# Optimization experiments

Hardware: AMD Instinct MI355X
Metric: run time of the kernel (lower is better)

The kernel has to match this reference:

```python
import jax, jax.numpy as jnp
import numpy as np

EPS = 1e-7
K = 15      # kernel_size
CIN = 128
F = 256


def setup_inputs() -> dict:
    key = jax.random.key(0)
    k1, k2 = jax.random.split(key)
    x = jax.random.normal(k1, (32, 4096, CIN), dtype=jnp.float32)
    # glorot-uniform init then UnitNorm over axes (0,1) per filter, matching the constraint
    limit = np.sqrt(6.0 / (K * CIN + F))
    kernel = jax.random.uniform(k2, (K, CIN, F), dtype=jnp.float32, minval=-limit, maxval=limit)
    kernel = kernel / jnp.sqrt(jnp.sum(kernel * kernel, axis=(0, 1), keepdims=True) + 1e-12)
    scale = jnp.full((1, 1, 1), 10.0, dtype=jnp.float32)
    bias = jnp.zeros((F,), dtype=jnp.float32)
    return {"inputs": x, "kernel": kernel, "scale": scale, "bias": bias}


def reference(inputs, kernel, scale, bias):
    # dot-product conv: (B, L-K+1, F), VALID padding, stride 1
    dot = jax.lax.conv_general_dilated(
        inputs, kernel, window_strides=(1,), padding="VALID",
        dimension_numbers=("NWC", "WIO", "NWC"))
    # sliding sum-of-squares over window*channels. In the original this is a
    # conv1d with an all-ones (K,CIN,F) kernel, i.e. every filter sees the same
    # scalar sum -> compute it once via a cumsum box filter and broadcast.
    k = kernel.shape[0]
    sq = jnp.sum(inputs * inputs, axis=-1)                       # (B, L)
    cs = jnp.cumsum(jnp.pad(sq, ((0, 0), (1, 0))), axis=1)       # (B, L+1)
    win = cs[:, k:] - cs[:, :-k]                                 # (B, L-K+1)
    norm_x = jnp.sqrt(win + EPS)[..., None]                      # (B, L-K+1, 1)
    return scale * (dot / norm_x) + bias
```

## Files before the change

### kernel.cpp

```cpp
#include <hip/hip_runtime.h>
#include <hip/hip_bf16.h>
#include <stdint.h>

#define K_TAPS 15
#define CIN    128
#define F_OUT  256
#define LSEQ   4096
#define LOUT   (LSEQ - K_TAPS + 1)
#define BATCH  32

typedef __attribute__((ext_vector_type(8))) short bf16x8;
typedef __attribute__((ext_vector_type(4))) float f32x4;

typedef __attribute__((address_space(1))) const unsigned int gu32_t;
typedef __attribute__((address_space(3))) unsigned int su32_t;

__global__ void prep_w_kernel(const float* __restrict__ W,
                              unsigned short* __restrict__ Wp) {
  int idx = blockIdx.x * 256 + threadIdx.x;
  int f  = idx & 255;
  int kc = idx >> 8;
  int c  = kc & 127;
  int k  = kc >> 7;
  float w = W[idx];
  __hip_bfloat16 hb = __float2bfloat16(w);
  int chalf = c >> 6;
  int c6    = c & 63;
  int slot  = ((c6 >> 3) ^ f) & 7;
  int cp    = slot * 8 + (c & 7);
  Wp[((size_t)(k * 2 + chalf) * 256 + f) * 64 + cp] =
      *reinterpret_cast<unsigned short*>(&hb);
}

__global__ void sq_kernel(const float* __restrict__ x, float* __restrict__ sq) {
  int wid  = threadIdx.x >> 6;
  int lane = threadIdx.x & 63;
  int half = lane >> 5;
  int lq   = lane & 31;
  long pos = (long)blockIdx.x * 8 + wid * 2 + half;
  const float4* xp = (const float4*)(x + pos * CIN) + lq;
  float4 v = *xp;
  float s = v.x * v.x + v.y * v.y + v.z * v.z + v.w * v.w;
  #pragma unroll
  for (int m = 1; m <= 16; m <<= 1) s += __shfl_xor(s, m, 64);
  if (lq == 0) sq[pos] = s;
}

__global__ void rn_kernel(const float* __restrict__ sq,
                          const float* __restrict__ scale,
                          float* __restrict__ rn) {
  int t = blockIdx.x * 256 + threadIdx.x;
  int b = blockIdx.y;
  if (t >= LOUT) return;
  const float* s = sq + b * LSEQ + t;
  float w = 0.f;
  #pragma unroll
  for (int k = 0; k < K_TAPS; ++k) w += s[k];
  rn[b * LSEQ + t] = scale[0] / sqrtf(w + 1e-7f);
}

#define BM 128
#define BN 128
#define XROWS 144
#define XBYTES (XROWS * 256)
#define BBYTES 16384
#define NPHASE (K_TAPS * 2)

__global__ __launch_bounds__(256, 2) void conv_gemm_kernel(
    const float* __restrict__ x, const unsigned short* __restrict__ Wp,
    const float* __restrict__ rn, const float* __restrict__ bias,
    float* __restrict__ out)
{
  __shared__ __align__(16) char lds[XBYTES + 2 * BBYTES];
  char* Xs = lds;
  char* Bs = lds + XBYTES;

  const int b     = blockIdx.y;
  const int mtile = blockIdx.x >> 1;
  const int ntile = blockIdx.x & 1;
  const int t0    = mtile * BM;
  const int n0    = ntile * BN;

  const int tx   = threadIdx.x;
  const int wid  = tx >> 6;
  const int lane = tx & 63;
  const int wm   = wid >> 1;
  const int wn   = wid & 1;

  {
    const int rloc = tx >> 4;
    const int g    = tx & 15;
    const float* xb = x + (long)b * LSEQ * CIN;
    #pragma unroll
    for (int it = 0; it < 9; ++it) {
      int row  = it * 16 + rloc;
      int grow = t0 + row;
      float v[8];
      if (grow < LSEQ) {
        const float4* p = (const float4*)(xb + (long)grow * CIN + g * 8);
        float4 a0 = p[0], a1 = p[1];
        v[0]=a0.x; v[1]=a0.y; v[2]=a0.z; v[3]=a0.w;
        v[4]=a1.x; v[5]=a1.y; v[6]=a1.z; v[7]=a1.w;
      } else {
        #pragma unroll
        for (int j = 0; j < 8; ++j) v[j] = 0.f;
      }
      union { unsigned short us[8]; int4 q; } pk;
      #pragma unroll
      for (int j = 0; j < 8; ++j) {
        __hip_bfloat16 hb = __float2bfloat16(v[j]);
        pk.us[j] = *reinterpret_cast<unsigned short*>(&hb);
      }
      int slot = (g & 8) | ((g ^ row) & 7);
      *(int4*)(Xs + row * 256 + slot * 16) = pk.q;
    }
  }

  auto stageB = [&](int buf, int phase) {
    const char* src = (const char*)Wp + (size_t)phase * 32768
                      + (size_t)n0 * 128;
    char* dst = Bs + buf * BBYTES;
    int base = wid * 4096;
    #pragma unroll
    for (int i = 0; i < 4; ++i) {
      int off = base + i * 1024;
      __builtin_amdgcn_global_load_lds(
          (gu32_t*)(src + off + lane * 16),
          (su32_t*)(dst + off), 16, 0, 0);
    }
  };

  stageB(0, 0);
  __syncthreads();

  f32x4 acc[4][4] = {};

  const int klane = lane >> 4;
  const int rl    = lane & 15;
  const int arow0 = wm * 64;
  const int bcol0 = wn * 64;

  for (int ph = 0; ph < NPHASE; ++ph) {
    int buf = ph & 1;
    if (ph + 1 < NPHASE) stageB(buf ^ 1, ph + 1);
    const char* Bsc = Bs + buf * BBYTES;
    const int tap = ph >> 1;
    const int kk0 = (ph & 1) * 2;
    #pragma unroll
    for (int j = 0; j < 2; ++j) {
      const int kk = kk0 + j;
      bf16x8 af[4], bfr[4];
      const int ga = kk * 4 + klane;
      const int gb = (kk & 1) * 4 + klane;
      #pragma unroll
      for (int mf = 0; mf < 4; ++mf) {
        int row  = arow0 + mf * 16 + rl + tap;
        int slot = (ga & 8) | ((ga ^ row) & 7);
        af[mf] = *(const bf16x8*)(Xs + row * 256 + slot * 16);
      }
      #pragma unroll
      for (int nf = 0; nf < 4; ++nf) {
        int fc   = bcol0 + nf * 16 + rl;
        int slot = (gb ^ fc) & 7;
        bfr[nf] = *(const bf16x8*)(Bsc + fc * 128 + slot * 16);
      }
      #pragma unroll
      for (int mf = 0; mf < 4; ++mf)
        #pragma unroll
        for (int nf = 0; nf < 4; ++nf)
          acc[mf][nf] = __builtin_amdgcn_mfma_f32_16x16x32_bf16(
              af[mf], bfr[nf], acc[mf][nf], 0, 0, 0);
    }
    __syncthreads();
  }

  const int rgrp = lane >> 4;
  float biasv[4];
  #pragma unroll
  for (int nf = 0; nf < 4; ++nf) biasv[nf] = bias[n0 + bcol0 + nf * 16 + rl];
  float* ob = out + (long)b * LOUT * F_OUT;
  const float* rnb = rn + b * LSEQ + t0;
  #pragma unroll
  for (int mf = 0; mf < 4; ++mf) {
    #pragma unroll
    for (int r = 0; r < 4; ++r) {
      int row = arow0 + mf * 16 + rgrp * 4 + r;
      int gt  = t0 + row;
      if (gt < LOUT) {
        float rv = rnb[row];
        #pragma unroll
        for (int nf = 0; nf < 4; ++nf) {
          ob[(long)gt * F_OUT + n0 + bcol0 + nf * 16 + rl] =
              acc[mf][nf][r] * rv + biasv[nf];
        }
      }
    }
  }
}

extern "C" void kernel_launch(void* const* d_in, const int* in_sizes, int n_in,
                              void* d_out, int out_size, void* d_ws, size_t ws_size,
                              hipStream_t stream) {
  const float* x     = (const float*)d_in[0];
  const float* W     = (const float*)d_in[1];
  const float* scale = (const float*)d_in[2];
  const float* bias  = (const float*)d_in[3];
  float* out = (float*)d_out;

  char* ws = (char*)d_ws;
  unsigned short* Wp = (unsigned short*)ws;
  float* sq = (float*)(ws + 1048576);
  float* rn = (float*)(ws + 1048576 + 524288);

  prep_w_kernel<<<1920, 256, 0, stream>>>(W, Wp);
  sq_kernel<<<BATCH * LSEQ / 8, 256, 0, stream>>>(x, sq);
  rn_kernel<<<dim3((LOUT + 255) / 256, BATCH), 256, 0, stream>>>(sq, scale, rn);
  conv_gemm_kernel<<<dim3(64, BATCH), 256, 0, stream>>>(x, Wp, rn, bias, out);
}
```

Baseline: 148.9 us.

## Load weight fragments directly from global into registers, drop LDS staging

Changes the packed-weight layout so each lane's MFMA B fragment is a contiguous 16-byte global load. Weights now go straight into registers with a two-phase register double buffer, instead of being staged through double-buffered LDS with per-phase barriers. This removes the per-phase __syncthreads and the B LDS traffic, and shrinks LDS so occupancy can rise to 3 blocks per SM. The cost is more register pressure and exposed global or L2 latency on the weight loads, which every wave now issues redundantly.

```diff
diff --git a/kernel.cpp b/kernel.cpp
--- a/kernel.cpp
+++ b/kernel.cpp
@@ -11,9 +11,6 @@
 
 typedef __attribute__((ext_vector_type(8))) short bf16x8;
 typedef __attribute__((ext_vector_type(4))) float f32x4;
-
-typedef __attribute__((address_space(1))) const unsigned int gu32_t;
-typedef __attribute__((address_space(3))) unsigned int su32_t;
 
 __global__ void prep_w_kernel(const float* __restrict__ W,
                               unsigned short* __restrict__ Wp) {
@@ -24,12 +21,11 @@
   int k  = kc >> 7;
   float w = W[idx];
   __hip_bfloat16 hb = __float2bfloat16(w);
-  int chalf = c >> 6;
-  int c6    = c & 63;
-  int slot  = ((c6 >> 3) ^ f) & 7;
-  int cp    = slot * 8 + (c & 7);
-  Wp[((size_t)(k * 2 + chalf) * 256 + f) * 64 + cp] =
-      *reinterpret_cast<unsigned short*>(&hb);
+  int kk = c >> 5;
+  int kl = (c >> 3) & 3;
+  int c7 = c & 7;
+  size_t o = ((((size_t)(k * 4 + kk) * 256 + f) * 4 + kl) * 8) + c7;
+  Wp[o] = *reinterpret_cast<unsigned short*>(&hb);
 }
 
 __global__ void sq_kernel(const float* __restrict__ x, float* __restrict__ sq) {
@@ -60,32 +56,33 @@
 }
 
 #define BM 128
-#define BN 128
 #define XROWS 144
 #define XBYTES (XROWS * 256)
-#define BBYTES 16384
 #define NPHASE (K_TAPS * 2)
 
-__global__ __launch_bounds__(256, 2) void conv_gemm_kernel(
+__global__ __launch_bounds__(256, 3) void conv_gemm_kernel(
     const float* __restrict__ x, const unsigned short* __restrict__ Wp,
     const float* __restrict__ rn, const float* __restrict__ bias,
     float* __restrict__ out)
 {
-  __shared__ __align__(16) char lds[XBYTES + 2 * BBYTES];
-  char* Xs = lds;
-  char* Bs = lds + XBYTES;
+  __shared__ __align__(16) char Xs[XBYTES];
 
   const int b     = blockIdx.y;
   const int mtile = blockIdx.x >> 1;
   const int ntile = blockIdx.x & 1;
   const int t0    = mtile * BM;
-  const int n0    = ntile * BN;
+  const int n0    = ntile * 128;
 
   const int tx   = threadIdx.x;
   const int wid  = tx >> 6;
   const int lane = tx & 63;
   const int wm   = wid >> 1;
   const int wn   = wid & 1;
+
+  const int klane = lane >> 4;
+  const int rl    = lane & 15;
+  const int arow0 = wm * 64;
+  const int bcol0 = wn * 64;
 
   {
     const int rloc = tx >> 4;
@@ -115,43 +112,33 @@
       *(int4*)(Xs + row * 256 + slot * 16) = pk.q;
     }
   }
-
-  auto stageB = [&](int buf, int phase) {
-    const char* src = (const char*)Wp + (size_t)phase * 32768
-                      + (size_t)n0 * 128;
-    char* dst = Bs + buf * BBYTES;
-    int base = wid * 4096;
-    #pragma unroll
-    for (int i = 0; i < 4; ++i) {
-      int off = base + i * 1024;
-      __builtin_amdgcn_global_load_lds(
-          (gu32_t*)(src + off + lane * 16),
-          (su32_t*)(dst + off), 16, 0, 0);
-    }
-  };
-
-  stageB(0, 0);
   __syncthreads();
 
-  f32x4 acc[4][4] = {};
-
-  const int klane = lane >> 4;
-  const int rl    = lane & 15;
-  const int arow0 = wm * 64;
-  const int bcol0 = wn * 64;
-
-  for (int ph = 0; ph < NPHASE; ++ph) {
-    int buf = ph & 1;
-    if (ph + 1 < NPHASE) stageB(buf ^ 1, ph + 1);
-    const char* Bsc = Bs + buf * BBYTES;
+  const char* wbase = (const char*)Wp
+      + (size_t)(n0 + bcol0 + rl) * 64 + (size_t)klane * 16;
+  auto loadB = [&](int ph, bf16x8* br) {
     const int tap = ph >> 1;
     const int kk0 = (ph & 1) * 2;
     #pragma unroll
     for (int j = 0; j < 2; ++j) {
+      const char* base = wbase + (size_t)((tap * 4 + kk0 + j) * 256) * 64;
+      #pragma unroll
+      for (int nf = 0; nf < 4; ++nf) {
+        br[j * 4 + nf] = *(const bf16x8*)(base + (size_t)nf * 16 * 64);
+      }
+    }
+  };
+
+  f32x4 acc[4][4] = {};
+
+  auto compute = [&](int ph, const bf16x8* br) {
+    const int tap = ph >> 1;
+    const int kk0 = (ph & 1) * 2;
+    #pragma unroll
+    for (int j = 0; j < 2; ++j) {
       const int kk = kk0 + j;
-      bf16x8 af[4], bfr[4];
       const int ga = kk * 4 + klane;
-      const int gb = (kk & 1) * 4 + klane;
+      bf16x8 af[4];
       #pragma unroll
       for (int mf = 0; mf < 4; ++mf) {
         int row  = arow0 + mf * 16 + rl + tap;
@@ -159,19 +146,22 @@
         af[mf] = *(const bf16x8*)(Xs + row * 256 + slot * 16);
       }
       #pragma unroll
-      for (int nf = 0; nf < 4; ++nf) {
-        int fc   = bcol0 + nf * 16 + rl;
-        int slot = (gb ^ fc) & 7;
-        bfr[nf] = *(const bf16x8*)(Bsc + fc * 128 + slot * 16);
-      }
-      #pragma unroll
       for (int mf = 0; mf < 4; ++mf)
         #pragma unroll
         for (int nf = 0; nf < 4; ++nf)
           acc[mf][nf] = __builtin_amdgcn_mfma_f32_16x16x32_bf16(
-              af[mf], bfr[nf], acc[mf][nf], 0, 0, 0);
-    }
-    __syncthreads();
+              af[mf], br[j * 4 + nf], acc[mf][nf], 0, 0, 0);
+    }
+  };
+
+  bf16x8 bA[8], bB[8];
+  loadB(0, bA);
+  #pragma unroll 3
+  for (int ph = 0; ph < NPHASE; ph += 2) {
+    loadB(ph + 1, bB);
+    compute(ph, bA);
+    if (ph + 2 < NPHASE) loadB(ph + 2, bA);
+    compute(ph + 1, bB);
   }
 
   const int rgrp = lane >> 4;
```

Result: slower. 169.2 us (+13.6%).

## Overlap weight prefetch with MFMA using manual vmcnt waits and split barriers

Applied to the files above, without the earlier changes.

Replaces the per-phase __syncthreads with explicit s_waitcnt vmcnt(4) and s_barrier, so the next phase's weight tile prefetch into LDS can stay in flight while the current phase's MFMAs run. The first weight-tile load is now issued before the input tile is converted to bf16 and staged, hiding its latency. A-fragment reads are hoisted ahead of the barrier, MFMAs are wrapped in s_setprio, and the phase loop is unrolled by 2. This relies on correct manual waitcnt accounting for the async LDS loads, which makes it fragile if the number of loads per stage changes.

```diff
diff --git a/kernel.cpp b/kernel.cpp
--- a/kernel.cpp
+++ b/kernel.cpp
@@ -87,6 +87,22 @@
   const int wm   = wid >> 1;
   const int wn   = wid & 1;
 
+  auto stageB = [&](int buf, int phase) {
+    const char* src = (const char*)Wp + (size_t)phase * 32768
+                      + (size_t)n0 * 128;
+    char* dst = Bs + buf * BBYTES;
+    int base = wid * 4096;
+    #pragma unroll
+    for (int i = 0; i < 4; ++i) {
+      int off = base + i * 1024;
+      __builtin_amdgcn_global_load_lds(
+          (gu32_t*)(src + off + lane * 16),
+          (su32_t*)(dst + off), 16, 0, 0);
+    }
+  };
+
+  stageB(0, 0);
+
   {
     const int rloc = tx >> 4;
     const int g    = tx & 15;
@@ -115,22 +131,6 @@
       *(int4*)(Xs + row * 256 + slot * 16) = pk.q;
     }
   }
-
-  auto stageB = [&](int buf, int phase) {
-    const char* src = (const char*)Wp + (size_t)phase * 32768
-                      + (size_t)n0 * 128;
-    char* dst = Bs + buf * BBYTES;
-    int base = wid * 4096;
-    #pragma unroll
-    for (int i = 0; i < 4; ++i) {
-      int off = base + i * 1024;
-      __builtin_amdgcn_global_load_lds(
-          (gu32_t*)(src + off + lane * 16),
-          (su32_t*)(dst + off), 16, 0, 0);
-    }
-  };
-
-  stageB(0, 0);
   __syncthreads();
 
   f32x4 acc[4][4] = {};
@@ -140,38 +140,59 @@
   const int arow0 = wm * 64;
   const int bcol0 = wn * 64;
 
+  #pragma unroll 2
   for (int ph = 0; ph < NPHASE; ++ph) {
-    int buf = ph & 1;
-    if (ph + 1 < NPHASE) stageB(buf ^ 1, ph + 1);
-    const char* Bsc = Bs + buf * BBYTES;
+    const int buf = ph & 1;
     const int tap = ph >> 1;
     const int kk0 = (ph & 1) * 2;
+
+    if (ph + 1 < NPHASE) stageB(buf ^ 1, ph + 1);
+
+    bf16x8 af[2][4];
     #pragma unroll
     for (int j = 0; j < 2; ++j) {
-      const int kk = kk0 + j;
-      bf16x8 af[4], bfr[4];
-      const int ga = kk * 4 + klane;
-      const int gb = (kk & 1) * 4 + klane;
+      const int ga = (kk0 + j) * 4 + klane;
       #pragma unroll
       for (int mf = 0; mf < 4; ++mf) {
         int row  = arow0 + mf * 16 + rl + tap;
         int slot = (ga & 8) | ((ga ^ row) & 7);
-        af[mf] = *(const bf16x8*)(Xs + row * 256 + slot * 16);
-      }
+        af[j][mf] = *(const bf16x8*)(Xs + row * 256 + slot * 16);
+      }
+    }
+
+    if (ph + 1 < NPHASE) {
+      asm volatile("s_waitcnt vmcnt(4)" ::: "memory");
+    } else {
+      asm volatile("s_waitcnt vmcnt(0)" ::: "memory");
+    }
+    __builtin_amdgcn_s_barrier();
+
+    const char* Bsc = Bs + buf * BBYTES;
+    bf16x8 bfr[2][4];
+    #pragma unroll
+    for (int j = 0; j < 2; ++j) {
+      const int gb = ((kk0 + j) & 1) * 4 + klane;
       #pragma unroll
       for (int nf = 0; nf < 4; ++nf) {
         int fc   = bcol0 + nf * 16 + rl;
         int slot = (gb ^ fc) & 7;
-        bfr[nf] = *(const bf16x8*)(Bsc + fc * 128 + slot * 16);
-      }
+        bfr[j][nf] = *(const bf16x8*)(Bsc + fc * 128 + slot * 16);
+      }
+    }
+
+    __builtin_amdgcn_s_setprio(1);
+    #pragma unroll
+    for (int j = 0; j < 2; ++j)
       #pragma unroll
       for (int mf = 0; mf < 4; ++mf)
         #pragma unroll
         for (int nf = 0; nf < 4; ++nf)
           acc[mf][nf] = __builtin_amdgcn_mfma_f32_16x16x32_bf16(
-              af[mf], bfr[nf], acc[mf][nf], 0, 0, 0);
-    }
-    __syncthreads();
+              af[j][mf], bfr[j][nf], acc[mf][nf], 0, 0, 0);
+    __builtin_amdgcn_s_setprio(0);
+
+    asm volatile("s_waitcnt lgkmcnt(0)" ::: "memory");
+    __builtin_amdgcn_s_barrier();
   }
 
   const int rgrp = lane >> 4;
```

New measurement: 147.5 us, median of 2. No clear change (-0.9%).

## Halve weight stage size, add manual waitcnt barriers and raise occupancy

Applied to the files above, without the earlier changes.

Repacks the bf16 weights into 32-channel quarter-phases with a new 4-slot XOR swizzle, halving each LDS B buffer and doubling the phase count. The main loop now issues the next weight prefetch, loads A fragments before waiting, and uses explicit vmcnt/lgkmcnt waits plus raw s_barrier instead of __syncthreads. It also raises MFMA priority with s_setprio and asks for 3 blocks per CU, and the first weight prefetch is issued before the x tile is converted so the two overlap. The aim is to hide global-to-LDS latency and improve occupancy. The cost is twice as many barriers per tap and a hand-tuned wait count that must match the number of outstanding loads.

```diff
diff --git a/kernel.cpp b/kernel.cpp
--- a/kernel.cpp
+++ b/kernel.cpp
@@ -24,11 +24,11 @@
   int k  = kc >> 7;
   float w = W[idx];
   __hip_bfloat16 hb = __float2bfloat16(w);
-  int chalf = c >> 6;
-  int c6    = c & 63;
-  int slot  = ((c6 >> 3) ^ f) & 7;
-  int cp    = slot * 8 + (c & 7);
-  Wp[((size_t)(k * 2 + chalf) * 256 + f) * 64 + cp] =
+  int q    = c >> 5;
+  int g    = (c >> 3) & 3;
+  int slot = (g ^ f ^ (f >> 2)) & 3;
+  int cp   = slot * 8 + (c & 7);
+  Wp[((size_t)(k * 4 + q) * 256 + f) * 32 + cp] =
       *reinterpret_cast<unsigned short*>(&hb);
 }
 
@@ -63,10 +63,10 @@
 #define BN 128
 #define XROWS 144
 #define XBYTES (XROWS * 256)
-#define BBYTES 16384
-#define NPHASE (K_TAPS * 2)
-
-__global__ __launch_bounds__(256, 2) void conv_gemm_kernel(
+#define BBYTES 8192
+#define NPHASE (K_TAPS * 4)
+
+__global__ __launch_bounds__(256, 3) void conv_gemm_kernel(
     const float* __restrict__ x, const unsigned short* __restrict__ Wp,
     const float* __restrict__ rn, const float* __restrict__ bias,
     float* __restrict__ out)
@@ -86,6 +86,22 @@
   const int lane = tx & 63;
   const int wm   = wid >> 1;
   const int wn   = wid & 1;
+
+  auto stageB = [&](int buf, int phase) {
+    const char* src = (const char*)Wp + (size_t)phase * 16384
+                      + (size_t)n0 * 64;
+    char* dst = Bs + buf * BBYTES;
+    int base = wid * 2048;
+    #pragma unroll
+    for (int i = 0; i < 2; ++i) {
+      int off = base + i * 1024;
+      __builtin_amdgcn_global_load_lds(
+          (gu32_t*)(src + off + lane * 16),
+          (su32_t*)(dst + off), 16, 0, 0);
+    }
+  };
+
+  stageB(0, 0);
 
   {
     const int rloc = tx >> 4;
@@ -115,22 +131,6 @@
       *(int4*)(Xs + row * 256 + slot * 16) = pk.q;
     }
   }
-
-  auto stageB = [&](int buf, int phase) {
-    const char* src = (const char*)Wp + (size_t)phase * 32768
-                      + (size_t)n0 * 128;
-    char* dst = Bs + buf * BBYTES;
-    int base = wid * 4096;
-    #pragma unroll
-    for (int i = 0; i < 4; ++i) {
-      int off = base + i * 1024;
-      __builtin_amdgcn_global_load_lds(
-          (gu32_t*)(src + off + lane * 16),
-          (su32_t*)(dst + off), 16, 0, 0);
-    }
-  };
-
-  stageB(0, 0);
   __syncthreads();
 
   f32x4 acc[4][4] = {};
@@ -140,38 +140,50 @@
   const int arow0 = wm * 64;
   const int bcol0 = wn * 64;
 
+  #pragma unroll 4
   for (int ph = 0; ph < NPHASE; ++ph) {
-    int buf = ph & 1;
+    const int buf = ph & 1;
+    const int tap = ph >> 2;
+    const int qtr = ph & 3;
+
     if (ph + 1 < NPHASE) stageB(buf ^ 1, ph + 1);
+
+    const int ga = qtr * 4 + klane;
+    bf16x8 af[4];
+    #pragma unroll
+    for (int mf = 0; mf < 4; ++mf) {
+      int row  = arow0 + mf * 16 + rl + tap;
+      int slot = (ga & 8) | ((ga ^ row) & 7);
+      af[mf] = *(const bf16x8*)(Xs + row * 256 + slot * 16);
+    }
+
+    if (ph + 1 < NPHASE) {
+      asm volatile("s_waitcnt vmcnt(2)" ::: "memory");
+    } else {
+      asm volatile("s_waitcnt vmcnt(0)" ::: "memory");
+    }
+    __builtin_amdgcn_s_barrier();
+
     const char* Bsc = Bs + buf * BBYTES;
-    const int tap = ph >> 1;
-    const int kk0 = (ph & 1) * 2;
-    #pragma unroll
-    for (int j = 0; j < 2; ++j) {
-      const int kk = kk0 + j;
-      bf16x8 af[4], bfr[4];
-      const int ga = kk * 4 + klane;
-      const int gb = (kk & 1) * 4 + klane;
+    bf16x8 bfr[4];
+    #pragma unroll
+    for (int nf = 0; nf < 4; ++nf) {
+      int fc   = bcol0 + nf * 16 + rl;
+      int slot = (klane ^ fc ^ (fc >> 2)) & 3;
+      bfr[nf] = *(const bf16x8*)(Bsc + fc * 64 + slot * 16);
+    }
+
+    __builtin_amdgcn_s_setprio(1);
+    #pragma unroll
+    for (int mf = 0; mf < 4; ++mf)
       #pragma unroll
-      for (int mf = 0; mf < 4; ++mf) {
-        int row  = arow0 + mf * 16 + rl + tap;
-        int slot = (ga & 8) | ((ga ^ row) & 7);
-        af[mf] = *(const bf16x8*)(Xs + row * 256 + slot * 16);
-      }
-      #pragma unroll
-      for (int nf = 0; nf < 4; ++nf) {
-        int fc   = bcol0 + nf * 16 + rl;
-        int slot = (gb ^ fc) & 7;
-        bfr[nf] = *(const bf16x8*)(Bsc + fc * 128 + slot * 16);
-      }
-      #pragma unroll
-      for (int mf = 0; mf < 4; ++mf)
-        #pragma unroll
-        for (int nf = 0; nf < 4; ++nf)
-          acc[mf][nf] = __builtin_amdgcn_mfma_f32_16x16x32_bf16(
-              af[mf], bfr[nf], acc[mf][nf], 0, 0, 0);
-    }
-    __syncthreads();
+      for (int nf = 0; nf < 4; ++nf)
+        acc[mf][nf] = __builtin_amdgcn_mfma_f32_16x16x32_bf16(
+            af[mf], bfr[nf], acc[mf][nf], 0, 0, 0);
+    __builtin_amdgcn_s_setprio(0);
+
+    asm volatile("s_waitcnt lgkmcnt(0)" ::: "memory");
+    __builtin_amdgcn_s_barrier();
   }
 
   const int rgrp = lane >> 4;
```

Measured after the change: 141.0 us. 5.3% less time.
